# Kernel optimization log

Hardware: AMD Instinct MI355X
Metric: run time of the kernel (lower is better)

The kernel has to match this reference:

```python
import jax, jax.numpy as jnp
import numpy as np

B, D, C = 16384, 512, 1000  # batch, feature dim, number of class prototypes


def setup_inputs() -> dict:
    key = jax.random.key(0)
    kx, kp = jax.random.split(key)
    x = jax.random.normal(kx, (B, D), dtype=jnp.float32)
    protomat = jax.random.normal(kp, (C, D), dtype=jnp.float32)
    return {"x": x, "protomat": protomat}


def reference(x, protomat):
    # Squared L2 distance from every sample to every prototype:
    # dist[b, c] = sum_d (x[b,d] - protomat[c,d])^2
    # materializing the [B, C, D] broadcast the original loop implies.
    x_sq = jnp.sum(x * x, axis=1, keepdims=True)            # [B, 1]
    p_sq = jnp.sum(protomat * protomat, axis=1)             # [C]
    cross = jnp.einsum('bd,cd->bc', x, protomat)            # [B, C]
    return x_sq + p_sq[None, :] - 2.0 * cross               # [B, C]
```

## Files before the change

kernel.cpp:

```cpp
#include <hip/hip_runtime.h>
#include <hip/hip_bf16.h>


#define B_ROWS 16384
#define D_K    512
#define C_COLS 1000
#define C_PAD  1024

#define BM 128
#define BN 128
#define BK 32
#define NK (D_K / BK)
#define NBUF 4

typedef __attribute__((ext_vector_type(8))) short short8;
typedef __attribute__((ext_vector_type(4))) float f32x4;

__device__ __forceinline__ unsigned short f2bf(float f) {
  unsigned u = __float_as_uint(f);
  u += 0x7fffu + ((u >> 16) & 1u);
  return (unsigned short)(u >> 16);
}

__device__ __forceinline__ void gload16(const void* g, void* l) {
  __builtin_amdgcn_global_load_lds(
      (const __attribute__((address_space(1))) unsigned int*)g,
      (__attribute__((address_space(3))) unsigned int*)l, 16, 0, 0);
}

__global__ __launch_bounds__(256) void prep_kernel(
    const float* __restrict__ x, const float* __restrict__ p,
    unsigned short* __restrict__ xb, unsigned short* __restrict__ pb,
    float* __restrict__ xsq, float* __restrict__ psq) {
  const int wave = threadIdx.x >> 6;
  const int lane = threadIdx.x & 63;
  const int row  = blockIdx.x * 4 + wave;
  const bool isx = row < B_ROWS;
  const int r2   = isx ? row : row - B_ROWS;

  float v[8];
  if (isx) {
    const float4* s = reinterpret_cast<const float4*>(x + (size_t)r2 * D_K + lane * 8);
    float4 a = s[0], b = s[1];
    v[0] = a.x; v[1] = a.y; v[2] = a.z; v[3] = a.w;
    v[4] = b.x; v[5] = b.y; v[6] = b.z; v[7] = b.w;
  } else if (r2 < C_COLS) {
    const float4* s = reinterpret_cast<const float4*>(p + (size_t)r2 * D_K + lane * 8);
    float4 a = s[0], b = s[1];
    v[0] = a.x; v[1] = a.y; v[2] = a.z; v[3] = a.w;
    v[4] = b.x; v[5] = b.y; v[6] = b.z; v[7] = b.w;
  } else {
#pragma unroll
    for (int j = 0; j < 8; ++j) v[j] = 0.0f;
  }

  float ss = 0.0f;
  unsigned short u[8];
#pragma unroll
  for (int j = 0; j < 8; ++j) { ss += v[j] * v[j]; u[j] = f2bf(v[j]); }

  uint4 pk;
  pk.x = (unsigned)u[0] | ((unsigned)u[1] << 16);
  pk.y = (unsigned)u[2] | ((unsigned)u[3] << 16);
  pk.z = (unsigned)u[4] | ((unsigned)u[5] << 16);
  pk.w = (unsigned)u[6] | ((unsigned)u[7] << 16);
  unsigned short* dst = (isx ? xb : pb) + (size_t)r2 * D_K + lane * 8;
  *reinterpret_cast<uint4*>(dst) = pk;

#pragma unroll
  for (int off = 32; off > 0; off >>= 1) ss += __shfl_down(ss, off);
  if (lane == 0) (isx ? xsq : psq)[r2] = ss;
}

__global__ __launch_bounds__(256, 2) void gemm_kernel(
    const unsigned short* __restrict__ xb, const unsigned short* __restrict__ pb,
    const float* __restrict__ xsq, const float* __restrict__ psq,
    float* __restrict__ out) {
  __shared__ __align__(16) unsigned short As[NBUF][BM * BK];
  __shared__ __align__(16) unsigned short Bs[NBUF][BN * BK];

  const int tid  = threadIdx.x;
  const int lane = tid & 63;
  const int wave = tid >> 6;
  const int wr   = wave >> 1;
  const int wc   = wave & 1;

  const int bid = blockIdx.x;
  const int tt  = (bid & 7) * 128 + (bid >> 3);
  const int bm  = tt >> 3;
  const int bn  = tt & 7;

  const int ch0 = tid;
  const int ch1 = tid + 256;
  const int r0  = ch0 >> 2, r1 = ch1 >> 2;
  const int kg0 = ((ch0 & 3) - (r0 >> 1)) & 3;
  const int kg1 = ((ch1 & 3) - (r1 >> 1)) & 3;
  const unsigned short* a0 = xb + ((size_t)bm * BM + r0) * D_K + kg0 * 8;
  const unsigned short* a1 = xb + ((size_t)bm * BM + r1) * D_K + kg1 * 8;
  const unsigned short* b0 = pb + ((size_t)bn * BN + r0) * D_K + kg0 * 8;
  const unsigned short* b1 = pb + ((size_t)bn * BN + r1) * D_K + kg1 * 8;

  f32x4 acc[4][4];
#pragma unroll
  for (int i = 0; i < 4; ++i)
#pragma unroll
    for (int j = 0; j < 4; ++j) acc[i][j] = (f32x4){0.f, 0.f, 0.f, 0.f};

  const int mrow = wr * 64 + (lane & 15);
  const int ncol = wc * 64 + (lane & 15);
  const int pslot = (((lane >> 4) + ((lane & 15) >> 1)) & 3);
  const int koffb = pslot * 8;

#define STAGE(T, BUF)                                   \
  do {                                                  \
    const int ko = (T)*BK;                              \
    gload16(a0 + ko, &As[BUF][ch0 * 8]);                \
    gload16(a1 + ko, &As[BUF][ch1 * 8]);                \
    gload16(b0 + ko, &Bs[BUF][ch0 * 8]);                \
    gload16(b1 + ko, &Bs[BUF][ch1 * 8]);                \
  } while (0)

#define COMPUTE(BUF)                                                          \
  do {                                                                        \
    short8 af[4], bfr[4];                                                     \
    _Pragma("unroll") for (int i = 0; i < 4; ++i)                             \
        af[i] = *reinterpret_cast<const short8*>(                             \
            &As[BUF][(mrow + i * 16) * BK + koffb]);                          \
    _Pragma("unroll") for (int j = 0; j < 4; ++j)                             \
        bfr[j] = *reinterpret_cast<const short8*>(                            \
            &Bs[BUF][(ncol + j * 16) * BK + koffb]);                          \
    _Pragma("unroll") for (int i = 0; i < 4; ++i)                             \
        _Pragma("unroll") for (int j = 0; j < 4; ++j)                         \
            acc[i][j] = __builtin_amdgcn_mfma_f32_16x16x32_bf16(              \
                af[i], bfr[j], acc[i][j], 0, 0, 0);                           \
  } while (0)

  STAGE(0, 0);
  STAGE(1, 1);

  for (int t = 0; t < NK - 2; ++t) {
    STAGE(t + 2, (t + 2) & 3);
    asm volatile("s_waitcnt vmcnt(8)" ::: "memory");
    __builtin_amdgcn_s_barrier();
    COMPUTE(t & 3);
  }
  asm volatile("s_waitcnt vmcnt(4)" ::: "memory");
  __builtin_amdgcn_s_barrier();
  COMPUTE((NK - 2) & 3);
  asm volatile("s_waitcnt vmcnt(0)" ::: "memory");
  __builtin_amdgcn_s_barrier();
  COMPUTE((NK - 1) & 3);

#undef STAGE
#undef COMPUTE

  const int colbase = bn * BN + wc * 64 + (lane & 15);
  float pc[4];
#pragma unroll
  for (int j = 0; j < 4; ++j) pc[j] = psq[colbase + j * 16];

  const int rowbase = bm * BM + wr * 64 + ((lane >> 4) << 2);
#pragma unroll
  for (int i = 0; i < 4; ++i) {
#pragma unroll
    for (int r = 0; r < 4; ++r) {
      const int row = rowbase + i * 16 + r;
      const float xs = xsq[row];
#pragma unroll
      for (int j = 0; j < 4; ++j) {
        const int c = colbase + j * 16;
        if (c < C_COLS)
          out[(size_t)row * C_COLS + c] = xs + pc[j] - 2.0f * acc[i][j][r];
      }
    }
  }
}

extern "C" void kernel_launch(void* const* d_in, const int* in_sizes, int n_in,
                              void* d_out, int out_size, void* d_ws, size_t ws_size,
                              hipStream_t stream) {
  const float* x = (const float*)d_in[0];
  const float* p = (const float*)d_in[1];
  float* out = (float*)d_out;

  char* ws = (char*)d_ws;
  unsigned short* xb  = (unsigned short*)ws;
  unsigned short* pb  = (unsigned short*)(ws + 16777216);
  float* xsq          = (float*)(ws + 16777216 + 1048576);
  float* psq          = (float*)(ws + 16777216 + 1048576 + 65536);

  prep_kernel<<<(B_ROWS + C_PAD) / 4, 256, 0, stream>>>(x, p, xb, pb, xsq, psq);

  gemm_kernel<<<1024, 256, 0, stream>>>(xb, pb, xsq, psq, out);
}
```

Baseline: 115.8 us.

## Enlarge GEMM tile to 256x256 with 8 waves and deeper prefetch

The block tile grows from 128x128 to 256x256 with 512 threads (8 waves in a 2x4 layout), each wave computing a 128x64 sub-tile that reuses B fragments across 8 A fragments. Prefetch distance goes from 2 to 3 stages in a single flat LDS buffer, the stage is issued after the barrier, and compute is wrapped in s_setprio. The aim is to raise arithmetic intensity and cut global and LDS traffic per MFMA. The trade-off is only 256 blocks on a 256-CU part, so roughly one block per CU, plus higher register pressure from 32 accumulators per wave.

```diff
diff --git a/kernel.cpp b/kernel.cpp
--- a/kernel.cpp
+++ b/kernel.cpp
@@ -7,11 +7,12 @@
 #define C_COLS 1000
 #define C_PAD  1024
 
-#define BM 128
-#define BN 128
+#define BM 256
+#define BN 256
 #define BK 32
 #define NK (D_K / BK)
 #define NBUF 4
+#define TILE_SH 16384
 
 typedef __attribute__((ext_vector_type(8))) short short8;
 typedef __attribute__((ext_vector_type(4))) float f32x4;
@@ -72,105 +73,115 @@
   if (lane == 0) (isx ? xsq : psq)[r2] = ss;
 }
 
-__global__ __launch_bounds__(256, 2) void gemm_kernel(
+__global__ __launch_bounds__(512, 2) void gemm_kernel(
     const unsigned short* __restrict__ xb, const unsigned short* __restrict__ pb,
     const float* __restrict__ xsq, const float* __restrict__ psq,
     float* __restrict__ out) {
-  __shared__ __align__(16) unsigned short As[NBUF][BM * BK];
-  __shared__ __align__(16) unsigned short Bs[NBUF][BN * BK];
+  __shared__ __align__(16) unsigned short L[NBUF * TILE_SH];
 
   const int tid  = threadIdx.x;
   const int lane = tid & 63;
   const int wave = tid >> 6;
-  const int wr   = wave >> 1;
-  const int wc   = wave & 1;
+  const int wm   = wave >> 2;
+  const int wn   = wave & 3;
 
   const int bid = blockIdx.x;
-  const int tt  = (bid & 7) * 128 + (bid >> 3);
-  const int bm  = tt >> 3;
-  const int bn  = tt & 7;
-
-  const int ch0 = tid;
-  const int ch1 = tid + 256;
-  const int r0  = ch0 >> 2, r1 = ch1 >> 2;
-  const int kg0 = ((ch0 & 3) - (r0 >> 1)) & 3;
-  const int kg1 = ((ch1 & 3) - (r1 >> 1)) & 3;
-  const unsigned short* a0 = xb + ((size_t)bm * BM + r0) * D_K + kg0 * 8;
-  const unsigned short* a1 = xb + ((size_t)bm * BM + r1) * D_K + kg1 * 8;
-  const unsigned short* b0 = pb + ((size_t)bn * BN + r0) * D_K + kg0 * 8;
-  const unsigned short* b1 = pb + ((size_t)bn * BN + r1) * D_K + kg1 * 8;
-
-  f32x4 acc[4][4];
-#pragma unroll
-  for (int i = 0; i < 4; ++i)
-#pragma unroll
-    for (int j = 0; j < 4; ++j) acc[i][j] = (f32x4){0.f, 0.f, 0.f, 0.f};
-
-  const int mrow = wr * 64 + (lane & 15);
-  const int ncol = wc * 64 + (lane & 15);
-  const int pslot = (((lane >> 4) + ((lane & 15) >> 1)) & 3);
-  const int koffb = pslot * 8;
-
-#define STAGE(T, BUF)                                   \
-  do {                                                  \
-    const int ko = (T)*BK;                              \
-    gload16(a0 + ko, &As[BUF][ch0 * 8]);                \
-    gload16(a1 + ko, &As[BUF][ch1 * 8]);                \
-    gload16(b0 + ko, &Bs[BUF][ch0 * 8]);                \
-    gload16(b1 + ko, &Bs[BUF][ch1 * 8]);                \
+  const int tt  = (bid & 7) * 32 + (bid >> 3);
+  const int bm  = tt >> 2;
+  const int bn  = tt & 3;
+
+  const int chA0 = tid, chA1 = tid + 512;
+  const int rA0 = chA0 >> 2, rA1 = chA1 >> 2;
+  const int ksA0 = ((chA0 & 3) - (rA0 >> 1)) & 3;
+  const int ksA1 = ((chA1 & 3) - (rA1 >> 1)) & 3;
+  const unsigned short* gA0 = xb + ((size_t)bm * BM + rA0) * D_K + ksA0 * 8;
+  const unsigned short* gA1 = xb + ((size_t)bm * BM + rA1) * D_K + ksA1 * 8;
+  const unsigned short* gB0 = pb + ((size_t)bn * BN + rA0) * D_K + ksA0 * 8;
+  const unsigned short* gB1 = pb + ((size_t)bn * BN + rA1) * D_K + ksA1 * 8;
+  unsigned short* lA0 = &L[chA0 * 8];
+  unsigned short* lA1 = &L[chA1 * 8];
+  unsigned short* lB0 = &L[8192 + chA0 * 8];
+  unsigned short* lB1 = &L[8192 + chA1 * 8];
+
+  f32x4 acc[8][4];
+#pragma unroll
+  for (int m = 0; m < 8; ++m)
+#pragma unroll
+    for (int n = 0; n < 4; ++n) acc[m][n] = (f32x4){0.f, 0.f, 0.f, 0.f};
+
+  const int l15 = lane & 15;
+  const int pos = (((lane >> 4) + (l15 >> 1)) & 3);
+  const int rdA = (wm * 128 + l15) * 32 + pos * 8;
+  const int rdB = 8192 + (wn * 64 + l15) * 32 + pos * 8;
+
+#define STAGE(T, BUF)                                     \
+  do {                                                    \
+    const int ko = (T)*BK;                                \
+    const int bo = (BUF)*TILE_SH;                         \
+    gload16(gA0 + ko, lA0 + bo);                          \
+    gload16(gA1 + ko, lA1 + bo);                          \
+    gload16(gB0 + ko, lB0 + bo);                          \
+    gload16(gB1 + ko, lB1 + bo);                          \
   } while (0)
 
 #define COMPUTE(BUF)                                                          \
   do {                                                                        \
-    short8 af[4], bfr[4];                                                     \
-    _Pragma("unroll") for (int i = 0; i < 4; ++i)                             \
-        af[i] = *reinterpret_cast<const short8*>(                             \
-            &As[BUF][(mrow + i * 16) * BK + koffb]);                          \
-    _Pragma("unroll") for (int j = 0; j < 4; ++j)                             \
-        bfr[j] = *reinterpret_cast<const short8*>(                            \
-            &Bs[BUF][(ncol + j * 16) * BK + koffb]);                          \
-    _Pragma("unroll") for (int i = 0; i < 4; ++i)                             \
-        _Pragma("unroll") for (int j = 0; j < 4; ++j)                         \
-            acc[i][j] = __builtin_amdgcn_mfma_f32_16x16x32_bf16(              \
-                af[i], bfr[j], acc[i][j], 0, 0, 0);                           \
+    const unsigned short* Ab = &L[(BUF)*TILE_SH] + rdA;                       \
+    const unsigned short* Bb = &L[(BUF)*TILE_SH] + rdB;                       \
+    short8 bfr[4];                                                            \
+    _Pragma("unroll") for (int n = 0; n < 4; ++n)                             \
+        bfr[n] = *reinterpret_cast<const short8*>(Bb + n * 512);              \
+    __builtin_amdgcn_s_setprio(1);                                            \
+    _Pragma("unroll") for (int m = 0; m < 8; ++m) {                           \
+      short8 af = *reinterpret_cast<const short8*>(Ab + m * 512);             \
+      _Pragma("unroll") for (int n = 0; n < 4; ++n)                           \
+          acc[m][n] = __builtin_amdgcn_mfma_f32_16x16x32_bf16(                \
+              af, bfr[n], acc[m][n], 0, 0, 0);                                \
+    }                                                                         \
+    __builtin_amdgcn_s_setprio(0);                                            \
   } while (0)
 
   STAGE(0, 0);
   STAGE(1, 1);
-
-  for (int t = 0; t < NK - 2; ++t) {
-    STAGE(t + 2, (t + 2) & 3);
+  STAGE(2, 2);
+
+#pragma unroll 1
+  for (int t = 0; t < NK - 3; ++t) {
     asm volatile("s_waitcnt vmcnt(8)" ::: "memory");
     __builtin_amdgcn_s_barrier();
+    STAGE(t + 3, (t + 3) & 3);
     COMPUTE(t & 3);
   }
+  asm volatile("s_waitcnt vmcnt(8)" ::: "memory");
+  __builtin_amdgcn_s_barrier();
+  COMPUTE(13 & 3);
   asm volatile("s_waitcnt vmcnt(4)" ::: "memory");
   __builtin_amdgcn_s_barrier();
-  COMPUTE((NK - 2) & 3);
+  COMPUTE(14 & 3);
   asm volatile("s_waitcnt vmcnt(0)" ::: "memory");
   __builtin_amdgcn_s_barrier();
-  COMPUTE((NK - 1) & 3);
+  COMPUTE(15 & 3);
 
 #undef STAGE
 #undef COMPUTE
 
-  const int colbase = bn * BN + wc * 64 + (lane & 15);
+  const int colb = bn * BN + wn * 64 + l15;
   float pc[4];
 #pragma unroll
-  for (int j = 0; j < 4; ++j) pc[j] = psq[colbase + j * 16];
-
-  const int rowbase = bm * BM + wr * 64 + ((lane >> 4) << 2);
-#pragma unroll
-  for (int i = 0; i < 4; ++i) {
+  for (int n = 0; n < 4; ++n) pc[n] = psq[colb + n * 16];
+
+  const int rowb = bm * BM + wm * 128 + ((lane >> 4) << 2);
+#pragma unroll
+  for (int m = 0; m < 8; ++m) {
 #pragma unroll
     for (int r = 0; r < 4; ++r) {
-      const int row = rowbase + i * 16 + r;
+      const int row = rowb + m * 16 + r;
       const float xs = xsq[row];
 #pragma unroll
-      for (int j = 0; j < 4; ++j) {
-        const int c = colbase + j * 16;
+      for (int n = 0; n < 4; ++n) {
+        const int c = colb + n * 16;
         if (c < C_COLS)
-          out[(size_t)row * C_COLS + c] = xs + pc[j] - 2.0f * acc[i][j][r];
+          out[(size_t)row * C_COLS + c] = xs + pc[n] - 2.0f * acc[m][n][r];
       }
     }
   }
@@ -191,5 +202,5 @@
 
   prep_kernel<<<(B_ROWS + C_PAD) / 4, 256, 0, stream>>>(x, p, xb, pb, xsq, psq);
 
-  gemm_kernel<<<1024, 256, 0, stream>>>(xb, pb, xsq, psq, out);
-}
+  gemm_kernel<<<256, 512, 0, stream>>>(xb, pb, xsq, psq, out);
+}
```

Result: faster. 111.1 us (-4.1%).
